# Optimization experiments

Hardware: AMD Instinct MI355X
Metric: run time of the kernel (lower is better)

The kernel has to match this reference:

```python
import jax, jax.numpy as jnp
import numpy as np

N, D, H = 8192, 1280, 16
K = D // H          # head_dim = 80
S = 16              # number of packed segments
L = N // S          # tokens per segment = 512
SCALE = K ** -0.5


def rotate_half(x):
    x1, x2 = jnp.split(x, 2, axis=-1)
    return jnp.concatenate([-x2, x1], axis=-1)


def setup_inputs() -> dict:
    key = jax.random.key(0)
    ks = jax.random.split(key, 4)
    # RoPE tables over head_dim, shared by all heads
    inv_freq = 1.0 / (10000.0 ** (jnp.arange(0, K, 2, dtype=jnp.float32) / K))
    freqs = jnp.outer(jnp.arange(N, dtype=jnp.float32), inv_freq)  # [N, K/2]
    emb = jnp.concatenate([freqs, freqs], axis=-1)                 # [N, K]
    return {
        "hidden_ND": jax.random.normal(ks[0], (N, D), jnp.float32),
        "cu_seqlens": jnp.arange(S + 1, dtype=jnp.int32) * L,      # equal-length segments
        "cos_NK": jnp.cos(emb),
        "sin_NK": jnp.sin(emb),
        "qkv_w": jax.random.normal(ks[1], (D, 3 * D), jnp.float32) * (D ** -0.5),
        "qkv_b": jnp.zeros((3 * D,), jnp.float32),
        "proj_w": jax.random.normal(ks[2], (D, D), jnp.float32) * (D ** -0.5),
        "proj_b": jnp.zeros((D,), jnp.float32),
    }


def reference(hidden_ND, cu_seqlens, cos_NK, sin_NK, qkv_w, qkv_b, proj_w, proj_b):
    n = hidden_ND.shape[0]
    qkv = (hidden_ND @ qkv_w + qkv_b).reshape(n, 3, H, K)
    q, k, v = qkv[:, 0], qkv[:, 1], qkv[:, 2]          # each [N, H, K]
    cos = cos_NK[:, None, :]
    sin = sin_NK[:, None, :]
    q = q * cos + rotate_half(q) * sin
    k = k * cos + rotate_half(k) * sin
    # Block-diagonal attention over equal-length segments defined by cu_seqlens.
    num_seqs = cu_seqlens.shape[0] - 1
    seg_len = n // num_seqs
    qs = q.reshape(num_seqs, seg_len, H, K)
    ks_ = k.reshape(num_seqs, seg_len, H, K)
    vs = v.reshape(num_seqs, seg_len, H, K)
    logits = jnp.einsum('slhk,smhk->shlm', qs, ks_) * SCALE   # [S, H, L, L]
    w = jax.nn.softmax(logits.astype(jnp.float32), axis=-1).astype(logits.dtype)
    out = jnp.einsum('shlm,smhk->slhk', w, vs).reshape(n, H * K)
    return out @ proj_w + proj_b
```

## Files before the change

kernel.cpp:

```cpp
#include <hip/hip_runtime.h>

#define LOG2E 1.44269504088896340736f
#define ATT_SCALE 0.11180339887498949f

typedef _Float16 half8 __attribute__((ext_vector_type(8)));
typedef _Float16 half4v __attribute__((ext_vector_type(4)));
typedef __fp16 fp16x2 __attribute__((ext_vector_type(2)));
typedef float f32x4 __attribute__((ext_vector_type(4)));

#define MFMA(a, b, c) __builtin_amdgcn_mfma_f32_16x16x32_f16((a), (b), (c), 0, 0, 0)

__device__ __forceinline__ void async16(const _Float16* g, _Float16* l) {
  __builtin_amdgcn_global_load_lds(
      (const __attribute__((address_space(1))) unsigned int*)g,
      (__attribute__((address_space(3))) unsigned int*)l,
      16, 0, 0);
}

#define FENCE() asm volatile("" ::: "memory")
#define PHB()                                   \
  do {                                          \
    FENCE();                                    \
    __builtin_amdgcn_s_barrier();               \
    FENCE();                                    \
  } while (0)

__global__ __launch_bounds__(256) void cvt_k(const float* __restrict__ in,
                                             _Float16* __restrict__ out, int n4) {
  int i = blockIdx.x * 256 + threadIdx.x;
  if (i < n4) {
    f32x4 v = ((const f32x4*)in)[i];
    half4v hv;
    hv[0] = (_Float16)v[0]; hv[1] = (_Float16)v[1];
    hv[2] = (_Float16)v[2]; hv[3] = (_Float16)v[3];
    ((half4v*)out)[i] = hv;
  }
}

__global__ __launch_bounds__(256) void transpose_cvt_k(const float* __restrict__ in,
                                                       _Float16* __restrict__ out,
                                                       int R, int C) {
  __shared__ float tile[32][33];
  const int tx = threadIdx.x & 31, ty = threadIdx.x >> 5;
  const int c0 = blockIdx.x * 32, r0 = blockIdx.y * 32;
#pragma unroll
  for (int i = 0; i < 32; i += 8)
    tile[ty + i][tx] = in[(size_t)(r0 + ty + i) * C + c0 + tx];
  __syncthreads();
#pragma unroll
  for (int i = 0; i < 32; i += 8)
    out[(size_t)(c0 + ty + i) * R + r0 + tx] = (_Float16)tile[tx][ty + i];
}

__global__ __launch_bounds__(512, 2) void gemm256_k(const _Float16* __restrict__ A,
                                                    const _Float16* __restrict__ BT,
                                                    const float* __restrict__ bias,
                                                    _Float16* __restrict__ Qf,
                                                    _Float16* __restrict__ Kf,
                                                    _Float16* __restrict__ VTf) {
  __shared__ _Float16 sA[2][2][128 * 64];
  __shared__ _Float16 sB[2][2][128 * 64];
  const int tid = threadIdx.x;
  const int wave = tid >> 6, lane = tid & 63;
  const int quad = lane >> 4, l16 = lane & 15;
  const int wm = wave >> 2, wn = wave & 3;
  const int bh = wn >> 1, brb = (wn & 1) * 64;
  const int KD = 1280, NT = 20;

  const int id = blockIdx.x;
  const int xcd = id & 7;
  const int qq = (id >> 3) & 3;
  const int tn = id >> 5;
  const int tm = xcd * 4 + qq;
  const int m0 = tm * 256, n0 = tn * 256;

  f32x4 acc[8][4] = {};

  auto stageA = [&](int buf, int half, int kt) {
#pragma unroll
    for (int c = 0; c < 2; ++c) {
      const int s = c * 512 + wave * 64 + lane;
      const int row = s >> 3;
      const int lg = (s & 7) ^ (row & 7);
      async16(A + (size_t)(m0 + half * 128 + row) * KD + kt * 64 + lg * 8,
              &sA[buf][half][(size_t)(c * 512 + wave * 64) * 8]);
    }
  };
  auto stageB = [&](int buf, int half, int kt) {
#pragma unroll
    for (int c = 0; c < 2; ++c) {
      const int s = c * 512 + wave * 64 + lane;
      const int row = s >> 3;
      const int lg = (s & 7) ^ (row & 7);
      async16(BT + (size_t)(n0 + half * 128 + row) * KD + kt * 64 + lg * 8,
              &sB[buf][half][(size_t)(c * 512 + wave * 64) * 8]);
    }
  };
  auto ldA = [&](half8* af, const _Float16* hp, int rh) {
#pragma unroll
    for (int i = 0; i < 4; ++i)
#pragma unroll
      for (int kk = 0; kk < 2; ++kk) {
        const int lrow = rh * 64 + i * 16 + l16;
        const int pg = (kk * 4 + quad) ^ (l16 & 7);
        af[i * 2 + kk] = *(const half8*)(hp + lrow * 64 + pg * 8);
      }
  };
  auto ldB = [&](half8* bf, const _Float16* hp, int ch) {
#pragma unroll
    for (int j = 0; j < 2; ++j)
#pragma unroll
      for (int kk = 0; kk < 2; ++kk) {
        const int brow = brb + ch * 32 + j * 16 + l16;
        const int pg = (kk * 4 + quad) ^ (l16 & 7);
        bf[j * 2 + kk] = *(const half8*)(hp + brow * 64 + pg * 8);
      }
  };
  auto mmaq = [&](int r, int c, const half8* af, const half8* bf) {
#pragma unroll
    for (int i = 0; i < 4; ++i)
#pragma unroll
      for (int j = 0; j < 2; ++j)
#pragma unroll
        for (int kk = 0; kk < 2; ++kk)
          acc[r * 4 + i][c * 2 + j] =
              MFMA(af[i * 2 + kk], bf[j * 2 + kk], acc[r * 4 + i][c * 2 + j]);
  };

  stageA(0, 0, 0); stageA(0, 1, 0);
  stageB(0, 0, 0); stageB(0, 1, 0);
  stageB(1, 0, 1); stageB(1, 1, 1);
  asm volatile("s_waitcnt vmcnt(4)" ::: "memory");

  half8 af[8], bf0[4], bf1[4];
#pragma unroll 2
  for (int t = 0; t < NT; ++t) {
    const int buf = t & 1;
    const _Float16* aH = &sA[0][0][0] + buf * (2 * 128 * 64) + wm * (128 * 64);
    const _Float16* bH = &sB[0][0][0] + buf * (2 * 128 * 64) + bh * (128 * 64);

    PHB();
    ldA(af, aH, 0);
    ldB(bf0, bH, 0);
    if (t + 1 < NT) stageA(buf ^ 1, 0, t + 1);
    __builtin_amdgcn_s_setprio(1);
    mmaq(0, 0, af, bf0);
    __builtin_amdgcn_s_setprio(0);

    PHB();
    ldB(bf1, bH, 1);
    if (t + 1 < NT) stageA(buf ^ 1, 1, t + 1);
    __builtin_amdgcn_s_setprio(1);
    mmaq(0, 1, af, bf1);
    __builtin_amdgcn_s_setprio(0);

    PHB();
    ldA(af, aH, 1);
    if (t + 2 < NT) stageB(buf, 0, t + 2);
    __builtin_amdgcn_s_setprio(1);
    mmaq(1, 1, af, bf1);
    __builtin_amdgcn_s_setprio(0);

    PHB();
    if (t + 2 < NT) stageB(buf, 1, t + 2);
    if (t == NT - 2)
      asm volatile("s_waitcnt vmcnt(0)" ::: "memory");
    else if (t < NT - 2)
      asm volatile("s_waitcnt vmcnt(4)" ::: "memory");
    __builtin_amdgcn_s_setprio(1);
    mmaq(1, 0, af, bf0);
    __builtin_amdgcn_s_setprio(0);
  }

#pragma unroll
  for (int ridx = 0; ridx < 8; ++ridx) {
#pragma unroll
    for (int cidx = 0; cidx < 4; ++cidx) {
      const int col = n0 + wn * 64 + cidx * 16 + l16;
      const float bv = bias[col];
      const int rowb = m0 + wm * 128 + ridx * 16 + quad * 4;
      const int which = col / 1280;
      const int rem = col - which * 1280;
      const int h = rem / 80;
      const int kk = rem - h * 80;
#pragma unroll
      for (int r = 0; r < 4; ++r) {
        const float v = acc[ridx][cidx][r] + bv;
        const int mrow = rowb + r;
        const int s = mrow >> 9, l = mrow & 511;
        const int shh = s * 16 + h;
        if (which == 0)
          Qf[((size_t)shh * 512 + l) * 96 + kk] = (_Float16)v;
        else if (which == 1)
          Kf[((size_t)shh * 512 + l) * 96 + kk] = (_Float16)v;
        else
          VTf[((size_t)shh * 80 + kk) * 512 + l] = (_Float16)v;
      }
    }
  }
}

__global__ __launch_bounds__(256) void gemm_k(const _Float16* __restrict__ A,
                                              const _Float16* __restrict__ BT,
                                              const float* __restrict__ bias,
                                              float* __restrict__ Out) {
  __shared__ _Float16 sA[2][2][128 * 64];
  __shared__ _Float16 sB[2][2][64 * 64];
  const int tid = threadIdx.x;
  const int wave = tid >> 6, lane = tid & 63;
  const int quad = lane >> 4, l16 = lane & 15;
  const int wm = wave >> 1, wn = wave & 1;
  const int KD = 1280, NT = 20;

  const int m0 = blockIdx.x * 256;
  const int n0 = blockIdx.y * 128;

  f32x4 acc[8][4] = {};

  auto stageA = [&](int buf, int half, int kt) {
#pragma unroll
    for (int c = 0; c < 4; ++c) {
      const int s = c * 256 + tid;
      const int row = s >> 3;
      const int lg = (s & 7) ^ (row & 7);
      async16(A + (size_t)(m0 + half * 128 + row) * KD + kt * 64 + lg * 8,
              &sA[buf][half][(size_t)(c * 256 + wave * 64) * 8]);
    }
  };
  auto stageB = [&](int buf, int kt) {
#pragma unroll
    for (int c = 0; c < 4; ++c) {
      const int s = c * 256 + tid;
      const int row = s >> 3;
      const int lg = (s & 7) ^ (row & 7);
      async16(BT + (size_t)(n0 + row) * KD + kt * 64 + lg * 8,
              &sB[buf][0][(size_t)(c * 256 + wave * 64) * 8]);
    }
  };
  auto ldA = [&](half8* af, const _Float16* hp, int rh) {
#pragma unroll
    for (int i = 0; i < 4; ++i)
#pragma unroll
      for (int kk = 0; kk < 2; ++kk) {
        const int lrow = rh * 64 + i * 16 + l16;
        const int pg = (kk * 4 + quad) ^ (l16 & 7);
        af[i * 2 + kk] = *(const half8*)(hp + lrow * 64 + pg * 8);
      }
  };
  auto ldB = [&](half8* bf, const _Float16* hp, int ch) {
#pragma unroll
    for (int j = 0; j < 2; ++j)
#pragma unroll
      for (int kk = 0; kk < 2; ++kk) {
        const int brow = ch * 32 + j * 16 + l16;
        const int pg = (kk * 4 + quad) ^ (l16 & 7);
        bf[j * 2 + kk] = *(const half8*)(hp + brow * 64 + pg * 8);
      }
  };
  auto mmaq = [&](int r, int c, const half8* af, const half8* bf) {
#pragma unroll
    for (int i = 0; i < 4; ++i)
#pragma unroll
      for (int j = 0; j < 2; ++j)
#pragma unroll
        for (int kk = 0; kk < 2; ++kk)
          acc[r * 4 + i][c * 2 + j] =
              MFMA(af[i * 2 + kk], bf[j * 2 + kk], acc[r * 4 + i][c * 2 + j]);
  };

  stageA(0, 0, 0); stageA(0, 1, 0);
  stageB(0, 0);
  stageB(1, 1);
  asm volatile("s_waitcnt vmcnt(4)" ::: "memory");

  half8 af[8], bf0[4], bf1[4];
#pragma unroll 2
  for (int t = 0; t < NT; ++t) {
    const int buf = t & 1;
    const _Float16* aH = &sA[0][0][0] + buf * (2 * 128 * 64) + wm * (128 * 64);
    const _Float16* bH = &sB[0][0][0] + buf * (2 * 64 * 64) + wn * (64 * 64);

    PHB();
    ldA(af, aH, 0);
    ldB(bf0, bH, 0);
    if (t + 1 < NT) stageA(buf ^ 1, 0, t + 1);
    __builtin_amdgcn_s_setprio(1);
    mmaq(0, 0, af, bf0);
    __builtin_amdgcn_s_setprio(0);

    PHB();
    ldB(bf1, bH, 1);
    if (t + 1 < NT) stageA(buf ^ 1, 1, t + 1);
    __builtin_amdgcn_s_setprio(1);
    mmaq(0, 1, af, bf1);
    __builtin_amdgcn_s_setprio(0);

    PHB();
    ldA(af, aH, 1);
    if (t + 2 < NT) stageB(buf, t + 2);
    __builtin_amdgcn_s_setprio(1);
    mmaq(1, 1, af, bf1);
    __builtin_amdgcn_s_setprio(0);

    PHB();
    if (t == NT - 2)
      asm volatile("s_waitcnt vmcnt(0)" ::: "memory");
    else if (t < NT - 2)
      asm volatile("s_waitcnt vmcnt(4)" ::: "memory");
    __builtin_amdgcn_s_setprio(1);
    mmaq(1, 0, af, bf0);
    __builtin_amdgcn_s_setprio(0);
  }

#pragma unroll
  for (int ridx = 0; ridx < 8; ++ridx) {
#pragma unroll
    for (int cidx = 0; cidx < 4; ++cidx) {
      const int col = n0 + wn * 64 + cidx * 16 + l16;
      const float bv = bias[col];
      const int rowb = m0 + wm * 128 + ridx * 16 + quad * 4;
#pragma unroll
      for (int r = 0; r < 4; ++r)
        Out[(size_t)(rowb + r) * 1280 + col] = acc[ridx][cidx][r] + bv;
    }
  }
}

__global__ __launch_bounds__(256) void rope_k(_Float16* __restrict__ Qf,
                                              _Float16* __restrict__ Kf,
                                              const float* __restrict__ cosNK,
                                              const float* __restrict__ sinNK) {
  const int gid = blockIdx.x * 256 + threadIdx.x;
  const int jt = gid % 10;
  const int row = gid / 10;
  const int qk = row >> 17;
  const int r = row & 131071;
  _Float16* buf = qk ? Kf : Qf;
  const int l = r & 511;
  const int s = r >> 13;
  const int t = s * 512 + l;
  const size_t base = (size_t)r * 96;
  const int j0 = jt * 4;

  half4v v1 = *(const half4v*)(buf + base + j0);
  half4v v2 = *(const half4v*)(buf + base + 40 + j0);
  f32x4 c1 = *(const f32x4*)(cosNK + (size_t)t * 80 + j0);
  f32x4 s1 = *(const f32x4*)(sinNK + (size_t)t * 80 + j0);
  f32x4 c2 = *(const f32x4*)(cosNK + (size_t)t * 80 + 40 + j0);
  f32x4 s2 = *(const f32x4*)(sinNK + (size_t)t * 80 + 40 + j0);
  half4v o1, o2;
#pragma unroll
  for (int e = 0; e < 4; ++e) {
    const float a = (float)v1[e], b = (float)v2[e];
    o1[e] = (_Float16)(a * c1[e] - b * s1[e]);
    o2[e] = (_Float16)(b * c2[e] + a * s2[e]);
  }
  *(half4v*)(buf + base + j0) = o1;
  *(half4v*)(buf + base + 40 + j0) = o2;
  if (jt < 2) {
    half8 z = {};
    *(half8*)(buf + base + 80 + jt * 8) = z;
  }
}

__global__ __launch_bounds__(256) void attn_k(const _Float16* __restrict__ Qf,
                                              const _Float16* __restrict__ Kf,
                                              const _Float16* __restrict__ VTf,
                                              _Float16* __restrict__ attnA) {
  __shared__ _Float16 sP[128 * 72];
  __shared__ _Float16 sK[64 * 104];
  __shared__ _Float16 sV[96 * 72];
  const int tid = threadIdx.x;
  const int wave = tid >> 6, lane = tid & 63;
  const int quad = lane >> 4, l16 = lane & 15;
  const int shh = blockIdx.x;
  const int qt = blockIdx.y;
  const int h = shh & 15;
  const int s = shh >> 4;

  const _Float16* Qb = Qf + ((size_t)shh * 512 + qt * 128) * 96;
  const _Float16* Kb0 = Kf + (size_t)shh * 512 * 96;
  const _Float16* Vb0 = VTf + (size_t)shh * 80 * 512;

  const _Float16 c1h = (_Float16)(ATT_SCALE * LOG2E);
  half8 qf[2][3];
#pragma unroll
  for (int rt = 0; rt < 2; ++rt)
#pragma unroll
    for (int ks = 0; ks < 3; ++ks) {
      half8 t = *(const half8*)(Qb + (size_t)(wave * 32 + rt * 16 + l16) * 96 +
                                ks * 32 + quad * 8);
#pragma unroll
      for (int e = 0; e < 8; ++e) t[e] *= c1h;
      qf[rt][ks] = t;
    }

  for (int idx = tid; idx < 16 * 72; idx += 256) sV[80 * 72 + idx] = (_Float16)1.f;

  f32x4 o[2][6] = {};

  for (int kc = 0; kc < 8; ++kc) {
    __syncthreads();
    const _Float16* Kb = Kb0 + (size_t)kc * 64 * 96;
#pragma unroll
    for (int c = 0; c < 4; ++c) {
      const int j = wave + 4 * c;
      if (j < 13) {
        const int off = j * 1024 + lane * 16;
        const int krow = off / 208;
        const int kcol = off - krow * 208;
        if (kcol < 192)
          async16(Kb + (size_t)krow * 96 + (kcol >> 1), &sK[j * 512]);
      }
    }
#pragma unroll
    for (int c = 0; c < 3; ++c) {
      const int j = wave + 4 * c;
      const int off = j * 1024 + lane * 16;
      const int vrow = off / 144;
      const int colb = off - vrow * 144;
      if (vrow < 80 && colb < 128)
        async16(Vb0 + (size_t)vrow * 512 + kc * 64 + (colb >> 1), &sV[j * 512]);
    }
    __syncthreads();

    f32x4 sacc[2][4] = {};
#pragma unroll
    for (int mt = 0; mt < 4; ++mt) {
#pragma unroll
      for (int ks = 0; ks < 3; ++ks) {
        half8 kb = *(const half8*)&sK[(mt * 16 + l16) * 104 + ks * 32 + quad * 8];
        sacc[0][mt] = MFMA(kb, qf[0][ks], sacc[0][mt]);
        sacc[1][mt] = MFMA(kb, qf[1][ks], sacc[1][mt]);
      }
    }

#pragma unroll
    for (int rt = 0; rt < 2; ++rt) {
#pragma unroll
      for (int mt = 0; mt < 4; ++mt) {
        union { fp16x2 h2[2]; half4v h4; } u;
        u.h2[0] = __builtin_amdgcn_cvt_pkrtz(
            __builtin_amdgcn_exp2f(sacc[rt][mt][0]),
            __builtin_amdgcn_exp2f(sacc[rt][mt][1]));
        u.h2[1] = __builtin_amdgcn_cvt_pkrtz(
            __builtin_amdgcn_exp2f(sacc[rt][mt][2]),
            __builtin_amdgcn_exp2f(sacc[rt][mt][3]));
        *(half4v*)&sP[(wave * 32 + rt * 16 + l16) * 72 + mt * 16 + quad * 4] = u.h4;
      }
    }

#pragma unroll
    for (int ks = 0; ks < 2; ++ks) {
      half8 pa[2];
      pa[0] = *(const half8*)&sP[(wave * 32 + 0 + l16) * 72 + ks * 32 + quad * 8];
      pa[1] = *(const half8*)&sP[(wave * 32 + 16 + l16) * 72 + ks * 32 + quad * 8];
#pragma unroll
      for (int ft = 0; ft < 6; ++ft) {
        half8 vb = *(const half8*)&sV[(ft * 16 + l16) * 72 + ks * 32 + quad * 8];
        o[0][ft] = MFMA(pa[0], vb, o[0][ft]);
        o[1][ft] = MFMA(pa[1], vb, o[1][ft]);
      }
    }
  }

#pragma unroll
  for (int rt = 0; rt < 2; ++rt) {
#pragma unroll
    for (int r = 0; r < 4; ++r) {
      const float inv = 1.0f / o[rt][5][r];
      const int token = s * 512 + qt * 128 + wave * 32 + rt * 16 + quad * 4 + r;
#pragma unroll
      for (int ft = 0; ft < 5; ++ft)
        attnA[(size_t)token * 1280 + h * 80 + ft * 16 + l16] =
            (_Float16)(o[rt][ft][r] * inv);
    }
  }
}

extern "C" void kernel_launch(void* const* d_in, const int* in_sizes, int n_in,
                              void* d_out, int out_size, void* d_ws, size_t ws_size,
                              hipStream_t stream) {
  (void)in_sizes; (void)n_in; (void)out_size; (void)ws_size;
  const float* hidden = (const float*)d_in[0];
  const float* cosNK = (const float*)d_in[2];
  const float* sinNK = (const float*)d_in[3];
  const float* qkv_w = (const float*)d_in[4];
  const float* qkv_b = (const float*)d_in[5];
  const float* proj_w = (const float*)d_in[6];
  const float* proj_b = (const float*)d_in[7];
  float* out = (float*)d_out;

  char* ws = (char*)d_ws;
  _Float16* hA    = (_Float16*)(ws);
  _Float16* wT    = (_Float16*)(ws + 20971520);
  _Float16* projT = (_Float16*)(ws + 30801920);
  _Float16* Qf    = (_Float16*)(ws + 34078720);
  _Float16* Kf    = (_Float16*)(ws + 59244544);
  _Float16* VTf   = (_Float16*)(ws + 84410368);
  _Float16* attnA = (_Float16*)(ws + 105381888);

  cvt_k<<<10240, 256, 0, stream>>>(hidden, hA, 2621440);
  transpose_cvt_k<<<dim3(120, 40), 256, 0, stream>>>(qkv_w, wT, 1280, 3840);
  transpose_cvt_k<<<dim3(40, 40), 256, 0, stream>>>(proj_w, projT, 1280, 1280);
  gemm256_k<<<480, 512, 0, stream>>>(hA, wT, qkv_b, Qf, Kf, VTf);
  rope_k<<<10240, 256, 0, stream>>>(Qf, Kf, cosNK, sinNK);
  attn_k<<<dim3(256, 4), 256, 0, stream>>>(Qf, Kf, VTf, attnA);
  gemm_k<<<dim3(32, 10), 256, 0, stream>>>(attnA, projT, proj_b, out);
}
```

Baseline: 358.8 us.

## Shrink projection GEMM tile to 128x128 with simple double-buffered loop

The output projection GEMM moves from 256x128 tiles to 128x128 tiles, so the grid grows from 320 to 640 blocks on a 256-CU device. The four-phase interleaved pipeline with split A/B staging is replaced by a plain double-buffer loop that issues the next tile's async loads, computes the current one, and then waits for all loads. The goal is better wave balance across CUs and fewer accumulator registers. In exchange, each K step does less arithmetic per load and the full vmcnt(0) wait plus barrier every iteration gives less load/compute overlap.

```diff
diff --git a/kernel.cpp b/kernel.cpp
--- a/kernel.cpp
+++ b/kernel.cpp
@@ -204,124 +204,89 @@
                                               const _Float16* __restrict__ BT,
                                               const float* __restrict__ bias,
                                               float* __restrict__ Out) {
-  __shared__ _Float16 sA[2][2][128 * 64];
-  __shared__ _Float16 sB[2][2][64 * 64];
+  __shared__ _Float16 sA[2][128 * 64];
+  __shared__ _Float16 sB[2][128 * 64];
   const int tid = threadIdx.x;
   const int wave = tid >> 6, lane = tid & 63;
   const int quad = lane >> 4, l16 = lane & 15;
   const int wm = wave >> 1, wn = wave & 1;
   const int KD = 1280, NT = 20;
 
-  const int m0 = blockIdx.x * 256;
+  const int m0 = blockIdx.x * 128;
   const int n0 = blockIdx.y * 128;
 
-  f32x4 acc[8][4] = {};
-
-  auto stageA = [&](int buf, int half, int kt) {
+  f32x4 acc[4][4] = {};
+
+  auto stage = [&](_Float16* dst, const _Float16* src, int rbase, int kt) {
 #pragma unroll
     for (int c = 0; c < 4; ++c) {
       const int s = c * 256 + tid;
       const int row = s >> 3;
       const int lg = (s & 7) ^ (row & 7);
-      async16(A + (size_t)(m0 + half * 128 + row) * KD + kt * 64 + lg * 8,
-              &sA[buf][half][(size_t)(c * 256 + wave * 64) * 8]);
-    }
-  };
-  auto stageB = [&](int buf, int kt) {
-#pragma unroll
-    for (int c = 0; c < 4; ++c) {
-      const int s = c * 256 + tid;
-      const int row = s >> 3;
-      const int lg = (s & 7) ^ (row & 7);
-      async16(BT + (size_t)(n0 + row) * KD + kt * 64 + lg * 8,
-              &sB[buf][0][(size_t)(c * 256 + wave * 64) * 8]);
-    }
-  };
-  auto ldA = [&](half8* af, const _Float16* hp, int rh) {
+      async16(src + (size_t)(rbase + row) * KD + kt * 64 + lg * 8,
+              dst + (size_t)(c * 256 + wave * 64) * 8);
+    }
+  };
+  auto ldA = [&](half8* af, const _Float16* hp) {
 #pragma unroll
     for (int i = 0; i < 4; ++i)
 #pragma unroll
       for (int kk = 0; kk < 2; ++kk) {
-        const int lrow = rh * 64 + i * 16 + l16;
+        const int lrow = wm * 64 + i * 16 + l16;
         const int pg = (kk * 4 + quad) ^ (l16 & 7);
         af[i * 2 + kk] = *(const half8*)(hp + lrow * 64 + pg * 8);
       }
   };
-  auto ldB = [&](half8* bf, const _Float16* hp, int ch) {
-#pragma unroll
-    for (int j = 0; j < 2; ++j)
+  auto ldB = [&](half8* bf, const _Float16* hp) {
+#pragma unroll
+    for (int j = 0; j < 4; ++j)
 #pragma unroll
       for (int kk = 0; kk < 2; ++kk) {
-        const int brow = ch * 32 + j * 16 + l16;
+        const int brow = wn * 64 + j * 16 + l16;
         const int pg = (kk * 4 + quad) ^ (l16 & 7);
         bf[j * 2 + kk] = *(const half8*)(hp + brow * 64 + pg * 8);
       }
   };
-  auto mmaq = [&](int r, int c, const half8* af, const half8* bf) {
-#pragma unroll
-    for (int i = 0; i < 4; ++i)
-#pragma unroll
-      for (int j = 0; j < 2; ++j)
-#pragma unroll
-        for (int kk = 0; kk < 2; ++kk)
-          acc[r * 4 + i][c * 2 + j] =
-              MFMA(af[i * 2 + kk], bf[j * 2 + kk], acc[r * 4 + i][c * 2 + j]);
-  };
-
-  stageA(0, 0, 0); stageA(0, 1, 0);
-  stageB(0, 0);
-  stageB(1, 1);
-  asm volatile("s_waitcnt vmcnt(4)" ::: "memory");
-
-  half8 af[8], bf0[4], bf1[4];
+
+  stage(&sA[0][0], A, m0, 0);
+  stage(&sB[0][0], BT, n0, 0);
+  asm volatile("s_waitcnt vmcnt(0)" ::: "memory");
+  PHB();
+
+  half8 af[8], bf[8];
 #pragma unroll 2
   for (int t = 0; t < NT; ++t) {
     const int buf = t & 1;
-    const _Float16* aH = &sA[0][0][0] + buf * (2 * 128 * 64) + wm * (128 * 64);
-    const _Float16* bH = &sB[0][0][0] + buf * (2 * 64 * 64) + wn * (64 * 64);
-
+    if (t + 1 < NT) {
+      stage(&sA[buf ^ 1][0], A, m0, t + 1);
+      stage(&sB[buf ^ 1][0], BT, n0, t + 1);
+    }
+    ldA(af, &sA[buf][0]);
+    ldB(bf, &sB[buf][0]);
+    __builtin_amdgcn_s_setprio(1);
+#pragma unroll
+    for (int i = 0; i < 4; ++i)
+#pragma unroll
+      for (int j = 0; j < 4; ++j)
+#pragma unroll
+        for (int kk = 0; kk < 2; ++kk)
+          acc[i][j] = MFMA(af[i * 2 + kk], bf[j * 2 + kk], acc[i][j]);
+    __builtin_amdgcn_s_setprio(0);
+    if (t + 1 < NT)
+      asm volatile("s_waitcnt vmcnt(0)" ::: "memory");
     PHB();
-    ldA(af, aH, 0);
-    ldB(bf0, bH, 0);
-    if (t + 1 < NT) stageA(buf ^ 1, 0, t + 1);
-    __builtin_amdgcn_s_setprio(1);
-    mmaq(0, 0, af, bf0);
-    __builtin_amdgcn_s_setprio(0);
-
-    PHB();
-    ldB(bf1, bH, 1);
-    if (t + 1 < NT) stageA(buf ^ 1, 1, t + 1);
-    __builtin_amdgcn_s_setprio(1);
-    mmaq(0, 1, af, bf1);
-    __builtin_amdgcn_s_setprio(0);
-
-    PHB();
-    ldA(af, aH, 1);
-    if (t + 2 < NT) stageB(buf, t + 2);
-    __builtin_amdgcn_s_setprio(1);
-    mmaq(1, 1, af, bf1);
-    __builtin_amdgcn_s_setprio(0);
-
-    PHB();
-    if (t == NT - 2)
-      asm volatile("s_waitcnt vmcnt(0)" ::: "memory");
-    else if (t < NT - 2)
-      asm volatile("s_waitcnt vmcnt(4)" ::: "memory");
-    __builtin_amdgcn_s_setprio(1);
-    mmaq(1, 0, af, bf0);
-    __builtin_amdgcn_s_setprio(0);
-  }
-
-#pragma unroll
-  for (int ridx = 0; ridx < 8; ++ridx) {
-#pragma unroll
-    for (int cidx = 0; cidx < 4; ++cidx) {
-      const int col = n0 + wn * 64 + cidx * 16 + l16;
+  }
+
+#pragma unroll
+  for (int i = 0; i < 4; ++i) {
+#pragma unroll
+    for (int j = 0; j < 4; ++j) {
+      const int col = n0 + wn * 64 + j * 16 + l16;
       const float bv = bias[col];
-      const int rowb = m0 + wm * 128 + ridx * 16 + quad * 4;
+      const int rowb = m0 + wm * 64 + i * 16 + quad * 4;
 #pragma unroll
       for (int r = 0; r < 4; ++r)
-        Out[(size_t)(rowb + r) * 1280 + col] = acc[ridx][cidx][r] + bv;
+        Out[(size_t)(rowb + r) * 1280 + col] = acc[i][j][r] + bv;
     }
   }
 }
@@ -506,5 +471,5 @@
   gemm256_k<<<480, 512, 0, stream>>>(hA, wT, qkv_b, Qf, Kf, VTf);
   rope_k<<<10240, 256, 0, stream>>>(Qf, Kf, cosNK, sinNK);
   attn_k<<<dim3(256, 4), 256, 0, stream>>>(Qf, Kf, VTf, attnA);
-  gemm_k<<<dim3(32, 10), 256, 0, stream>>>(attnA, projT, proj_b, out);
-}
+  gemm_k<<<dim3(64, 10), 256, 0, stream>>>(attnA, projT, proj_b, out);
+}
```

After: 339.3 us. -5.4%, faster.
